# Performance work log

Hardware: AMD Instinct MI355X
Metric: run time of the kernel (lower is better)

## Reference

```python
import jax, jax.numpy as jnp
import numpy as np

HEADS = 16
WINDOW = 256
D_MODEL = 1024


def _ln(x, g, b, eps=1e-5):
    m = jnp.mean(x, -1, keepdims=True)
    var = jnp.mean((x - m) ** 2, -1, keepdims=True)
    return (x - m) * jax.lax.rsqrt(var + eps) * g + b


def _proj(x, g, b, W, bias):
    # torch: nn.Sequential(LayerNorm(d), Linear(d, h))
    return _ln(x, g, b) @ W.T + bias


def _bucket(x, pad_value):
    # x: (..., L, d) -> (..., nb, window, d), seq padded to multiple of window with pad_value
    L = x.shape[-2]
    n = WINDOW * (-(-L // WINDOW))
    pads = [(0, 0)] * x.ndim
    pads[-2] = (0, n - L)
    x = jnp.pad(x, pads, constant_values=pad_value)
    return x.reshape(*x.shape[:-2], n // WINDOW, WINDOW, x.shape[-1])


def _unfold(x, pad_value):
    # x: (..., nb, w, d) -> (..., nb, 2w, d): previous bucket (pad_value for bucket 0) || current
    pads = [(0, 0)] * x.ndim
    pads[-3] = (1, 0)
    prev = jnp.pad(x, pads, constant_values=pad_value)[..., :-1, :, :]
    return jnp.concatenate([prev, x], axis=-2)


def _rotary(x):
    # lucidrains rotary_embedding_torch default: theta=10000, interleaved pairs, positions 0..S-1 along dim -2
    S, d = x.shape[-2], x.shape[-1]
    inv = 1.0 / (10000.0 ** (jnp.arange(0, d, 2, dtype=jnp.float32) / d))
    freqs = jnp.arange(S, dtype=jnp.float32)[:, None] * inv[None, :]  # (S, d/2)
    freqs = jnp.repeat(freqs, 2, axis=-1)  # (S, d)
    cos, sin = jnp.cos(freqs).astype(x.dtype), jnp.sin(freqs).astype(x.dtype)
    xp = x.reshape(*x.shape[:-1], d // 2, 2)
    xr = jnp.stack([-xp[..., 1], xp[..., 0]], axis=-1).reshape(x.shape)
    return x * cos + xr * sin


def _forward(q, k, v, cell,
             ln_q_w, ln_q_b, w_q, b_q,
             ln_k_w, ln_k_b, w_k, b_k,
             ln_v_w, ln_v_b, w_v, b_v,
             ln_o_w, ln_o_b, w_o, b_o):
    B, L, D = q.shape
    hd = D // HEADS

    def split_heads(x):  # (B, L, D) -> (B, H, L, hd)
        return x.reshape(B, L, HEADS, hd).transpose(0, 2, 1, 3)

    qh = split_heads(_proj(q, ln_q_w, ln_q_b, w_q, b_q))
    kh = split_heads(_proj(k, ln_k_w, ln_k_b, w_k, b_k))
    vh = split_heads(_proj(v, ln_v_w, ln_v_b, w_v, b_v))

    bq = _bucket(qh, -1.0)                 # (B, H, nb, w, hd)
    bk = _unfold(_bucket(kh, -1.0), -1.0)  # (B, H, nb, 2w, hd)
    bv = _unfold(_bucket(vh, -1.0), -1.0)

    nb = bq.shape[2]
    n = nb * WINDOW
    i = _bucket(jnp.arange(n, dtype=jnp.int32)[:, None], -1)   # (nb, w, 1)
    j = jnp.swapaxes(_unfold(i, -1), -1, -2)                    # (nb, 1, 2w)
    mask = (i >= j) & (j != -1)                                 # (nb, w, 2w) causal + left pad
    req = _bucket(cell, -1)                                     # (B, 1, nb, w, 1)
    rek = jnp.swapaxes(_unfold(req, -1), -1, -2)                # (B, 1, nb, 1, 2w)
    mask = mask & (req == rek)                                  # (B, 1, nb, w, 2w)

    bq = _rotary(bq)
    bk = _rotary(bk)

    p = jnp.einsum('bhnqd,bhnkd->bhnqk', bq, bk) / jnp.sqrt(jnp.asarray(hd, bq.dtype))
    p = jnp.where(mask, p, jnp.finfo(p.dtype).min)
    a = jax.nn.softmax(p, axis=-1)
    o = jnp.einsum('bhnqk,bhnkd->bhnqd', a, bv)   # (B, H, nb, w, hd)
    o = o.reshape(B, HEADS, n, hd)[:, :, :L]      # drop seq padding
    o = o.transpose(0, 2, 1, 3).reshape(B, L, D)  # merge heads
    return _proj(o, ln_o_w, ln_o_b, w_o, b_o)


def setup_inputs() -> dict:
    key = jax.random.key(0)
    ks = jax.random.split(key, 10)
    B, L, D = 2, 4096, D_MODEL
    inp = {
        'q': jax.random.normal(ks[0], (B, L, D), dtype=jnp.float32),
        'k': jax.random.normal(ks[1], (B, L, D), dtype=jnp.float32),
        'v': jax.random.normal(ks[2], (B, L, D), dtype=jnp.float32),
        'cell': jnp.sort(jax.random.randint(ks[3], (B, 1, L, 1), 0, 64, dtype=jnp.int32), axis=2),
    }
    for idx, name in enumerate(['q', 'k', 'v', 'o']):
        inp[f'ln_{name}_w'] = jnp.ones((D,), jnp.float32)
        inp[f'ln_{name}_b'] = jnp.zeros((D,), jnp.float32)
        inp[f'w_{name}'] = jax.random.normal(ks[4 + idx], (D, D), dtype=jnp.float32) * 0.02
        inp[f'b_{name}'] = jnp.zeros((D,), jnp.float32)
    return inp


def reference(q, k, v, cell,
              ln_q_w, ln_q_b, w_q, b_q,
              ln_k_w, ln_k_b, w_k, b_k,
              ln_v_w, ln_v_b, w_v, b_v,
              ln_o_w, ln_o_b, w_o, b_o):
    return _forward(q, k, v, cell,
                    ln_q_w, ln_q_b, w_q, b_q,
                    ln_k_w, ln_k_b, w_k, b_k,
                    ln_v_w, ln_v_b, w_v, b_v,
                    ln_o_w, ln_o_b, w_o, b_o)
```

## Files before the change

kernel.cpp:

```cpp
#include <hip/hip_runtime.h>

#define HEADS 16
#define HD 64
#define DM 1024
#define LSEQ 4096
#define NEGF (-1.0e30f)

typedef __attribute__((ext_vector_type(8))) short bf16x8;
typedef __attribute__((ext_vector_type(4))) float f32x4;
typedef unsigned short u16;

#define MFMA16(a, b, c) __builtin_amdgcn_mfma_f32_16x16x32_bf16((a), (b), (c), 0, 0, 0)

static __device__ __forceinline__ float b2f(u16 u) {
  union { float f; unsigned i; } t; t.i = ((unsigned)u) << 16; return t.f;
}
static __device__ __forceinline__ u16 f2b(float f) {
  union { float f; unsigned i; } t; t.f = f;
  unsigned r = t.i + 0x7fffu + ((t.i >> 16) & 1u);
  return (u16)(r >> 16);
}
static __device__ __forceinline__ ushort4 pk4(float4 v) {
  return make_ushort4(f2b(v.x), f2b(v.y), f2b(v.z), f2b(v.w));
}
static __device__ __forceinline__ void gload16(const void* g, void* l) {
  __builtin_amdgcn_global_load_lds((const __attribute__((address_space(1))) void*)g,
                                   (__attribute__((address_space(3))) void*)l, 16, 0, 0);
}

__global__ __launch_bounds__(256) void prep(
    const float4* __restrict__ q, const float4* __restrict__ k, const float4* __restrict__ v,
    const float* __restrict__ g0, const float* __restrict__ b0,
    const float* __restrict__ g1, const float* __restrict__ b1,
    const float* __restrict__ g2, const float* __restrict__ b2,
    ushort4* __restrict__ o0, ushort4* __restrict__ o1, ushort4* __restrict__ o2,
    const float4* __restrict__ w0, const float4* __restrict__ w1,
    const float4* __restrict__ w2, const float4* __restrict__ w3,
    ushort4* __restrict__ wout,
    float* __restrict__ ropc, float* __restrict__ rops,
    const float* __restrict__ g3, const float* __restrict__ b3,
    const float* __restrict__ bias_o,
    float* __restrict__ c1, float* __restrict__ c2b) {
  __shared__ float ps[8];
  const int bid = blockIdx.x, tid = threadIdx.x;
  const int lane = tid & 63, wave = tid >> 6;
  if (bid < 24576) {
    const int row = bid & 8191, sel = bid >> 13;
    const float4* src = (sel == 0) ? q : (sel == 1) ? k : v;
    const float* gam = (sel == 0) ? g0 : (sel == 1) ? g1 : g2;
    const float* bet = (sel == 0) ? b0 : (sel == 1) ? b1 : b2;
    ushort4* dst = (sel == 0) ? o0 : (sel == 1) ? o1 : o2;

    float4 v4 = src[(size_t)row * 256 + tid];
    float s = v4.x + v4.y + v4.z + v4.w;
    float s2 = v4.x * v4.x + v4.y * v4.y + v4.z * v4.z + v4.w * v4.w;
#pragma unroll
    for (int d = 1; d < 64; d <<= 1) { s += __shfl_xor(s, d); s2 += __shfl_xor(s2, d); }
    if (lane == 0) { ps[wave] = s; ps[4 + wave] = s2; }
    __syncthreads();
    float tot = ps[0] + ps[1] + ps[2] + ps[3];
    float tot2 = ps[4] + ps[5] + ps[6] + ps[7];
    float mean = tot * (1.f / 1024.f);
    float var = tot2 * (1.f / 1024.f) - mean * mean;
    float rstd = rsqrtf(var + 1e-5f);
    float4 gv = ((const float4*)gam)[tid];
    float4 bv = ((const float4*)bet)[tid];
    dst[(size_t)row * 256 + tid] = make_ushort4(
        f2b((v4.x - mean) * rstd * gv.x + bv.x), f2b((v4.y - mean) * rstd * gv.y + bv.y),
        f2b((v4.z - mean) * rstd * gv.z + bv.z), f2b((v4.w - mean) * rstd * gv.w + bv.w));
  } else if (bid < 25600) {
    int i = (bid - 24576) * 256 + tid;
    wout[i]          = pk4(w0[i]);
    wout[i + 262144] = pk4(w1[i]);
    wout[i + 524288] = pk4(w2[i]);
    float4 wv = w3[i];
    float4 g4 = ((const float4*)g3)[i & 255];
    wv.x *= g4.x; wv.y *= g4.y; wv.z *= g4.z; wv.w *= g4.w;
    wout[i + 786432] = pk4(wv);
  } else if (bid < 25728) {
    int idx = (bid - 25600) * 256 + tid;
    int p = idx >> 6, d = idx & 63;
    int t2 = d & ~1;
    double inv = pow(10000.0, -(double)t2 / 64.0);
    double f = (double)p * inv;
    ropc[idx] = (float)cos(f);
    rops[idx] = (float)sin(f);
  } else {
    int n = bid - 25728;
    float4 wv = w3[n * 256 + tid];
    float4 gv = ((const float4*)g3)[tid];
    float4 bv = ((const float4*)b3)[tid];
    float s1 = wv.x * gv.x + wv.y * gv.y + wv.z * gv.z + wv.w * gv.w;
    float s2 = wv.x * bv.x + wv.y * bv.y + wv.z * bv.z + wv.w * bv.w;
#pragma unroll
    for (int d = 1; d < 64; d <<= 1) { s1 += __shfl_xor(s1, d); s2 += __shfl_xor(s2, d); }
    if (lane == 0) { ps[wave] = s1; ps[4 + wave] = s2; }
    __syncthreads();
    if (tid == 0) {
      c1[n] = ps[0] + ps[1] + ps[2] + ps[3];
      c2b[n] = ps[4] + ps[5] + ps[6] + ps[7] + bias_o[n];
    }
  }
}

__global__ __launch_bounds__(256) void ostats(const ushort4* __restrict__ xin,
                                              float* __restrict__ mean,
                                              float* __restrict__ rstd) {
  __shared__ float ps[8];
  int row = blockIdx.x, tid = threadIdx.x;
  int lane = tid & 63, wave = tid >> 6;
  ushort4 u = xin[(size_t)row * 256 + tid];
  float x = b2f(u.x), y = b2f(u.y), z = b2f(u.z), w = b2f(u.w);
  float s = x + y + z + w;
  float s2 = x * x + y * y + z * z + w * w;
#pragma unroll
  for (int d = 1; d < 64; d <<= 1) { s += __shfl_xor(s, d); s2 += __shfl_xor(s2, d); }
  if (lane == 0) { ps[wave] = s; ps[4 + wave] = s2; }
  __syncthreads();
  if (tid == 0) {
    float tot = ps[0] + ps[1] + ps[2] + ps[3];
    float tot2 = ps[4] + ps[5] + ps[6] + ps[7];
    float m = tot * (1.f / 1024.f);
    float var = tot2 * (1.f / 1024.f) - m * m;
    mean[row] = m;
    rstd[row] = rsqrtf(var + 1e-5f);
  }
}

__global__ __launch_bounds__(256, 3) void gemm_qkv(
    const u16* __restrict__ Aq, const u16* __restrict__ Ak, const u16* __restrict__ Av,
    const u16* __restrict__ wbf,
    const float* __restrict__ bq, const float* __restrict__ bk, const float* __restrict__ bv,
    const float* __restrict__ ropc, const float* __restrict__ rops,
    u16* __restrict__ qrot, u16* __restrict__ krot, u16* __restrict__ vTp) {
  __shared__ __align__(16) char smem[34816];
  u16* Als = (u16*)smem;
  u16* Bls = (u16*)(smem + 16384);
  const int tid = threadIdx.x, lane = tid & 63, wave = tid >> 6;
  const int g = lane >> 4, ln15 = lane & 15;
  const int mode = blockIdx.y;
  const u16* A = (mode == 0) ? Aq : (mode == 1) ? Ak : Av;
  const u16* Bw = wbf + (size_t)mode * 1048576;
  const float* bias = (mode == 0) ? bq : (mode == 1) ? bk : bv;
  const int bid = blockIdx.x;
  const int xcd = bid & 7, idx = bid >> 3;
  const int row0 = (xcd * 8 + (idx >> 3)) * 128;
  const int col0 = (idx & 7) * 128;
  const int wm = (wave >> 1) * 64, wn = (wave & 1) * 64;
  const int K = 1024;
  f32x4 acc[4][4] = {};

  for (int k0 = 0; k0 < K; k0 += 64) {
#pragma unroll
    for (int i = 0; i < 4; ++i) {
      int ch = i * 4 + wave;
      int olin = ch * 1024 + lane * 16;
      int r = olin >> 7;
      int cel = ((olin ^ ((r & 7) << 4)) >> 1) & 63;
      gload16(A + (size_t)(row0 + r) * K + k0 + cel, (char*)Als + ch * 1024);
    }
#pragma unroll
    for (int i = 0; i < 4; ++i) {
      int ch = i * 4 + wave;
      int olin = ch * 1024 + lane * 16;
      int r = olin >> 7;
      int cel = ((olin ^ ((r & 7) << 4)) >> 1) & 63;
      gload16(Bw + (size_t)(col0 + r) * K + k0 + cel, (char*)Bls + ch * 1024);
    }
    __syncthreads();
#pragma unroll
    for (int ks = 0; ks < 2; ++ks) {
      bf16x8 af[4], bfv[4];
      int cb = (ks * 32 + g * 8) * 2;
#pragma unroll
      for (int mi = 0; mi < 4; ++mi) {
        int r = wm + mi * 16 + ln15;
        af[mi] = *(const bf16x8*)((const char*)Als + r * 128 + (cb ^ ((r & 7) << 4)));
      }
#pragma unroll
      for (int ni = 0; ni < 4; ++ni) {
        int r = wn + ni * 16 + ln15;
        bfv[ni] = *(const bf16x8*)((const char*)Bls + r * 128 + (cb ^ ((r & 7) << 4)));
      }
#pragma unroll
      for (int mi = 0; mi < 4; ++mi)
#pragma unroll
        for (int ni = 0; ni < 4; ++ni)
          acc[mi][ni] = MFMA16(af[mi], bfv[ni], acc[mi][ni]);
    }
    __syncthreads();
  }

  u16* Cl = (u16*)smem;
#pragma unroll
  for (int mi = 0; mi < 4; ++mi)
#pragma unroll
    for (int ni = 0; ni < 4; ++ni)
#pragma unroll
      for (int r = 0; r < 4; ++r) {
        int rowc = wm + mi * 16 + g * 4 + r;
        int colc = wn + ni * 16 + ln15;
        int row = row0 + rowc, col = col0 + colc;
        float val = acc[mi][ni][r] + bias[col];
        if (mode == 2) {
          Cl[colc * 136 + rowc] = f2b(val);
        } else {
          if (mode == 0) val *= 0.125f;
          float oth = __shfl_xor(val, 1);
          int d = col & 63;
          int pp = (row & 255) + ((mode == 1) ? 256 : 0);
          float cc = ropc[pp * 64 + d], ss = rops[pp * 64 + d];
          Cl[rowc * 136 + colc] = f2b((d & 1) ? (val * cc + oth * ss) : (val * cc - oth * ss));
        }
      }
  __syncthreads();
  if (mode == 2) {
#pragma unroll
    for (int i = 0; i < 8; ++i) {
      int c2 = i * 256 + tid;
      int dloc = c2 >> 4, lgrp = c2 & 15;
      bf16x8 vv = *(const bf16x8*)(Cl + dloc * 136 + lgrp * 8);
      int colg = col0 + dloc, hh = colg >> 6, d = colg & 63;
      int l = row0 + lgrp * 8, bb = l >> 12, ll = l & 4095;
      *(bf16x8*)(vTp + (((size_t)bb * HEADS + hh) * HD + d) * LSEQ + ll) = vv;
    }
  } else {
    u16* dst = (mode == 0) ? qrot : krot;
#pragma unroll
    for (int i = 0; i < 8; ++i) {
      int c2 = i * 256 + tid;
      int rowc = c2 >> 4, cgrp = c2 & 15;
      bf16x8 vv = *(const bf16x8*)(Cl + rowc * 136 + cgrp * 8);
      int l = row0 + rowc, bb = l >> 12, ll = l & 4095;
      int colg = col0 + cgrp * 8, hh = colg >> 6, d0 = colg & 63;
      *(bf16x8*)(dst + (((size_t)bb * HEADS + hh) * LSEQ + ll) * HD + d0) = vv;
    }
  }
}

__global__ __launch_bounds__(256, 3) void gemm_o(
    const u16* __restrict__ A, const u16* __restrict__ Bw,
    const float* __restrict__ mean, const float* __restrict__ rstd,
    const float* __restrict__ c1, const float* __restrict__ c2b,
    float* __restrict__ outf) {
  __shared__ __align__(16) u16 Als[128 * 64];
  __shared__ __align__(16) u16 Bls[128 * 64];
  const int tid = threadIdx.x, lane = tid & 63, wave = tid >> 6;
  const int g = lane >> 4, ln15 = lane & 15;
  const int bid = blockIdx.x;
  const int xcd = bid & 7, idx = bid >> 3;
  const int row0 = (xcd * 8 + (idx >> 3)) * 128;
  const int col0 = (idx & 7) * 128;
  const int wm = (wave >> 1) * 64, wn = (wave & 1) * 64;
  const int K = 1024, N = 1024;
  f32x4 acc[4][4] = {};

  for (int k0 = 0; k0 < K; k0 += 64) {
#pragma unroll
    for (int i = 0; i < 4; ++i) {
      int ch = i * 4 + wave;
      int olin = ch * 1024 + lane * 16;
      int r = olin >> 7;
      int cel = ((olin ^ ((r & 7) << 4)) >> 1) & 63;
      gload16(A + (size_t)(row0 + r) * K + k0 + cel, (char*)Als + ch * 1024);
    }
#pragma unroll
    for (int i = 0; i < 4; ++i) {
      int ch = i * 4 + wave;
      int olin = ch * 1024 + lane * 16;
      int r = olin >> 7;
      int cel = ((olin ^ ((r & 7) << 4)) >> 1) & 63;
      gload16(Bw + (size_t)(col0 + r) * K + k0 + cel, (char*)Bls + ch * 1024);
    }
    __syncthreads();
#pragma unroll
    for (int ks = 0; ks < 2; ++ks) {
      bf16x8 af[4], bfv[4];
      int cb = (ks * 32 + g * 8) * 2;
#pragma unroll
      for (int mi = 0; mi < 4; ++mi) {
        int r = wm + mi * 16 + ln15;
        af[mi] = *(const bf16x8*)((const char*)Als + r * 128 + (cb ^ ((r & 7) << 4)));
      }
#pragma unroll
      for (int ni = 0; ni < 4; ++ni) {
        int r = wn + ni * 16 + ln15;
        bfv[ni] = *(const bf16x8*)((const char*)Bls + r * 128 + (cb ^ ((r & 7) << 4)));
      }
#pragma unroll
      for (int mi = 0; mi < 4; ++mi)
#pragma unroll
        for (int ni = 0; ni < 4; ++ni)
          acc[mi][ni] = MFMA16(af[mi], bfv[ni], acc[mi][ni]);
    }
    __syncthreads();
  }

#pragma unroll
  for (int mi = 0; mi < 4; ++mi)
#pragma unroll
    for (int r = 0; r < 4; ++r) {
      int row = row0 + wm + mi * 16 + g * 4 + r;
      float rho = rstd[row];
      float rm = rho * mean[row];
#pragma unroll
      for (int ni = 0; ni < 4; ++ni) {
        int col = col0 + wn + ni * 16 + ln15;
        outf[(size_t)row * N + col] = rho * acc[mi][ni][r] - rm * c1[col] + c2b[col];
      }
    }
}

__global__ __launch_bounds__(512, 2) void attn_kernel(
    const u16* __restrict__ qrot,
    const u16* __restrict__ krot,
    const u16* __restrict__ vT,
    const int* __restrict__ cell,
    const float* __restrict__ ropc, const float* __restrict__ rops,
    u16* __restrict__ o) {
  __shared__ __align__(16) u16 Kc[2][128 * 64];
  __shared__ __align__(16) u16 Pl[8 * 32 * 64];
  __shared__ int ci[256];
  __shared__ int cj[512];

  const int tid = threadIdx.x, lane = tid & 63, wave = tid >> 6;
  const int g = lane >> 4, ln15 = lane & 15;
  const int bucket = blockIdx.x & 15;
  const int h = (blockIdx.x >> 4) & 15;
  const int b = blockIdx.x >> 8;
  const int w0 = bucket * 256;
  const size_t base = (size_t)(b * HEADS + h) * LSEQ * HD;

  if (tid < 256) ci[tid] = cell[b * LSEQ + w0 + tid];
  {
    int gj = w0 - 256 + tid;
    cj[tid] = (gj >= 0) ? cell[b * LSEQ + gj] : (int)0x80000000;
  }

  bf16x8 qf[2][2];
#pragma unroll
  for (int mi = 0; mi < 2; ++mi)
#pragma unroll
    for (int ks = 0; ks < 2; ++ks)
      qf[mi][ks] = *(const bf16x8*)(qrot + base +
          (size_t)(w0 + wave * 32 + mi * 16 + ln15) * HD + ks * 32 + g * 8);

  bf16x8 qfB[2][2];
#pragma unroll
  for (int ks = 0; ks < 2; ++ks) {
    const int d0 = ks * 32 + g * 8;
    float rc[8], rs8[8];
#pragma unroll
    for (int j = 0; j < 8; ++j) {
      rc[j] = ropc[256 * 64 + d0 + j];
      rs8[j] = rops[256 * 64 + d0 + j];
    }
#pragma unroll
    for (int mi = 0; mi < 2; ++mi) {
      bf16x8 s = qf[mi][ks], t;
#pragma unroll
      for (int j = 0; j < 8; j += 2) {
        float e = b2f((u16)s[j]), od = b2f((u16)s[j + 1]);
        t[j]     = (short)f2b(e * rc[j] - od * rs8[j]);
        t[j + 1] = (short)f2b(e * rs8[j] + od * rc[j]);
      }
      qfB[mi][ks] = t;
    }
  }

  f32x4 Oa[2][4] = {};
  float mrow[2][4], lrow[2][4];
#pragma unroll
  for (int a1 = 0; a1 < 2; ++a1)
#pragma unroll
    for (int a2 = 0; a2 < 4; ++a2) { mrow[a1][a2] = NEGF; lrow[a1][a2] = 0.f; }

#define STAGE_K(bi, s)                                                          \
  {                                                                             \
    int gj0_ = w0 - 256 + (s) * 128;                                            \
    _Pragma("unroll")                                                           \
    for (int i_ = 0; i_ < 2; ++i_) {                                            \
      int ch_ = i_ * 8 + wave;                                                  \
      int olin_ = ch_ * 1024 + lane * 16;                                       \
      int r_ = olin_ >> 7;                                                      \
      int cel_ = ((olin_ ^ ((r_ & 7) << 4)) >> 1) & 63;                         \
      gload16(krot + base + (size_t)(gj0_ + r_) * HD + cel_,                    \
              (char*)Kc[bi] + ch_ * 1024);                                      \
    }                                                                           \
  }

  const int s0 = (bucket == 0) ? 2 : 0;
  STAGE_K(0, s0);
  __syncthreads();

  const int crb_lo = ci[0], crb_hi = ci[255];
  const int crw_lo = ci[wave * 32], crw_hi = ci[wave * 32 + 31];

  for (int s = s0; s < 4; ++s) {
    const int cur = (s - s0) & 1;
    if (s + 1 < 4) {
      int k1 = (s + 1) * 2;
      bool need = false;
#pragma unroll
      for (int kk = 0; kk < 2; ++kk) {
        int clo = cj[(k1 + kk) * 64], chi = cj[(k1 + kk) * 64 + 63];
        need = need || !(chi < crb_lo || clo > crb_hi);
      }
      if (need) STAGE_K(cur ^ 1, s + 1);
    }

#pragma unroll
    for (int sub = 0; sub < 2; ++sub) {
      const int k = s * 2 + sub;
      if (k * 64 > wave * 32 + 287) continue;
      {
        int clo = cj[k * 64], chi = cj[k * 64 + 63];
        if (chi < crw_lo || clo > crw_hi) continue;
      }
      const int gj0 = w0 - 256 + k * 64;
      const int lr0 = sub * 64;
      const bool prevhalf = (k < 4);

      bf16x8 vb[2][4];
#pragma unroll
      for (int jb = 0; jb < 2; ++jb)
#pragma unroll
        for (int nd = 0; nd < 4; ++nd) {
          int d = nd * 16 + ln15;
          int p0 = gj0 + jb * 32 + g * 8;
          vb[jb][nd] = *(const bf16x8*)(vT + base + (size_t)d * LSEQ + p0);
        }

#pragma unroll
      for (int mi = 0; mi < 2; ++mi) {
        f32x4 sc[4] = {};
        __builtin_amdgcn_s_setprio(1);
#pragma unroll
        for (int ks = 0; ks < 2; ++ks) {
          int cb = (ks * 32 + g * 8) * 2;
          bf16x8 aq = prevhalf ? qfB[mi][ks] : qf[mi][ks];
#pragma unroll
          for (int ni = 0; ni < 4; ++ni) {
            int r = lr0 + ni * 16 + ln15;
            bf16x8 kf = *(const bf16x8*)((const char*)Kc[cur] + r * 128 + (cb ^ ((r & 7) << 4)));
            sc[ni] = MFMA16(aq, kf, sc[ni]);
          }
        }
        __builtin_amdgcn_s_setprio(0);
        float mx[4] = {NEGF, NEGF, NEGF, NEGF};
#pragma unroll
        for (int ni = 0; ni < 4; ++ni)
#pragma unroll
          for (int r = 0; r < 4; ++r) {
            int iloc = wave * 32 + mi * 16 + g * 4 + r;
            int p = k * 64 + ni * 16 + ln15;
            bool ok = (p <= iloc + 256) && (ci[iloc] == cj[p]);
            float sv = ok ? sc[ni][r] : NEGF;
            sc[ni][r] = sv;
            mx[r] = fmaxf(mx[r], sv);
          }
#pragma unroll
        for (int d = 1; d < 16; d <<= 1)
#pragma unroll
          for (int r = 0; r < 4; ++r) mx[r] = fmaxf(mx[r], __shfl_xor(mx[r], d));
        float rs[4] = {0.f, 0.f, 0.f, 0.f};
        bool big = false;
#pragma unroll
        for (int r = 0; r < 4; ++r) big = big || (mx[r] > mrow[mi][r] + 8.0f);
        if (__any(big)) {
#pragma unroll
          for (int r = 0; r < 4; ++r) {
            float mold = mrow[mi][r];
            float mnew = fmaxf(mold, mx[r]);
            float alpha = __expf(mold - mnew);
            mrow[mi][r] = mnew;
            lrow[mi][r] *= alpha;
#pragma unroll
            for (int nd = 0; nd < 4; ++nd) Oa[mi][nd][r] *= alpha;
          }
        }
#pragma unroll
        for (int ni = 0; ni < 4; ++ni)
#pragma unroll
          for (int r = 0; r < 4; ++r) {
            float sv = sc[ni][r];
            float p = (sv > NEGF * 0.5f) ? __expf(sv - mrow[mi][r]) : 0.f;
            rs[r] += p;
            int row = mi * 16 + g * 4 + r;
            int colb = (ni * 16 + ln15) * 2;
            *(u16*)((char*)Pl + wave * 4096 + row * 128 + (colb ^ ((row & 7) << 4))) = f2b(p);
          }
#pragma unroll
        for (int d = 1; d < 16; d <<= 1)
#pragma unroll
          for (int r = 0; r < 4; ++r) rs[r] += __shfl_xor(rs[r], d);
#pragma unroll
        for (int r = 0; r < 4; ++r) lrow[mi][r] += rs[r];
      }

#pragma unroll
      for (int jb = 0; jb < 2; ++jb) {
        bf16x8 pa[2];
        int cb = (jb * 32 + g * 8) * 2;
#pragma unroll
        for (int mi = 0; mi < 2; ++mi) {
          int row = mi * 16 + ln15;
          pa[mi] = *(const bf16x8*)((const char*)Pl + wave * 4096 + row * 128 + (cb ^ ((row & 7) << 4)));
        }
        __builtin_amdgcn_s_setprio(1);
#pragma unroll
        for (int mi = 0; mi < 2; ++mi)
#pragma unroll
          for (int nd = 0; nd < 4; ++nd) Oa[mi][nd] = MFMA16(pa[mi], vb[jb][nd], Oa[mi][nd]);
        __builtin_amdgcn_s_setprio(0);
      }
    }

    __syncthreads();
  }

#pragma unroll
  for (int mi = 0; mi < 2; ++mi)
#pragma unroll
    for (int r = 0; r < 4; ++r) {
      float invl = 1.0f / lrow[mi][r];
      int gi = w0 + wave * 32 + mi * 16 + g * 4 + r;
      size_t ob = ((size_t)b * LSEQ + gi) * DM + h * HD;
#pragma unroll
      for (int nd = 0; nd < 4; ++nd) o[ob + nd * 16 + ln15] = f2b(Oa[mi][nd][r] * invl);
    }
#undef STAGE_K
}

extern "C" void kernel_launch(void* const* d_in, const int* in_sizes, int n_in,
                              void* d_out, int out_size, void* d_ws, size_t ws_size,
                              hipStream_t stream) {
  const float* q = (const float*)d_in[0];
  const float* k = (const float*)d_in[1];
  const float* v = (const float*)d_in[2];
  const int* cell = (const int*)d_in[3];
  const float* lnw[4] = {(const float*)d_in[4], (const float*)d_in[8], (const float*)d_in[12], (const float*)d_in[16]};
  const float* lnb[4] = {(const float*)d_in[5], (const float*)d_in[9], (const float*)d_in[13], (const float*)d_in[17]};
  const float* Wm[4]  = {(const float*)d_in[6], (const float*)d_in[10], (const float*)d_in[14], (const float*)d_in[18]};
  const float* bi[4]  = {(const float*)d_in[7], (const float*)d_in[11], (const float*)d_in[15], (const float*)d_in[19]};

  char* ws = (char*)d_ws;
  u16* xlnq  = (u16*)(ws);
  u16* wbf   = (u16*)(ws + 16777216);
  u16* qrot  = (u16*)(ws + 25165824);
  u16* krot  = (u16*)(ws + 41943040);
  float* omean = (float*)(ws + 58720256);
  float* orstd = (float*)(ws + 58753024);
  float* c1    = (float*)(ws + 58785792);
  float* c2b   = (float*)(ws + 58789888);
  u16* vT    = (u16*)(ws + 75497472);
  u16* obuf  = (u16*)(ws + 92274688);
  float* ropc = (float*)(ws + 109051904);
  float* rops = (float*)(ws + 109182976);
  u16* xlnk = obuf;
  u16* xlnv = (u16*)d_out;

  prep<<<26752, 256, 0, stream>>>(
      (const float4*)q, (const float4*)k, (const float4*)v,
      lnw[0], lnb[0], lnw[1], lnb[1], lnw[2], lnb[2],
      (ushort4*)xlnq, (ushort4*)xlnk, (ushort4*)xlnv,
      (const float4*)Wm[0], (const float4*)Wm[1], (const float4*)Wm[2], (const float4*)Wm[3],
      (ushort4*)wbf, ropc, rops,
      lnw[3], lnb[3], bi[3], c1, c2b);

  dim3 gq(512, 3);
  gemm_qkv<<<gq, 256, 0, stream>>>(xlnq, xlnk, xlnv, wbf, bi[0], bi[1], bi[2],
                                   ropc, rops, qrot, krot, vT);
  attn_kernel<<<512, 512, 0, stream>>>(qrot, krot, vT, cell, ropc, rops, obuf);
  ostats<<<8192, 256, 0, stream>>>((const ushort4*)obuf, omean, orstd);
  gemm_o<<<512, 256, 0, stream>>>(obuf, wbf + 3145728, omean, orstd, c1, c2b, (float*)d_out);
}
```

Baseline: 191.4 us.

## Split attention blocks into half-buckets, load K directly, compute row sums via MFMA

The attention kernel now launches 1024 blocks of 256 threads, each covering half a query bucket, with a blockIdx remap that groups neighbouring blocks. K is read straight from global memory instead of being double-buffered in LDS, which removes the per-stage barriers and frees shared memory for more resident blocks. The softmax switches to exp2 with log2(e) folded into the query scale. Row sums come from an extra MFMA against a vector of ones instead of shuffle reductions. The risks are redundant K/V traffic across the two halves and uncoalesced direct global K fragment loads.

```diff
diff --git a/kernel.cpp b/kernel.cpp
--- a/kernel.cpp
+++ b/kernel.cpp
@@ -205,7 +205,7 @@
         if (mode == 2) {
           Cl[colc * 136 + rowc] = f2b(val);
         } else {
-          if (mode == 0) val *= 0.125f;
+          if (mode == 0) val *= 0.18033688011112042f;
           float oth = __shfl_xor(val, 1);
           int d = col & 63;
           int pp = (row & 255) + ((mode == 1) ? 256 : 0);
@@ -311,31 +311,38 @@
     }
 }
 
-__global__ __launch_bounds__(512, 2) void attn_kernel(
+__global__ __launch_bounds__(256, 4) void attn_kernel(
     const u16* __restrict__ qrot,
     const u16* __restrict__ krot,
     const u16* __restrict__ vT,
     const int* __restrict__ cell,
     const float* __restrict__ ropc, const float* __restrict__ rops,
     u16* __restrict__ o) {
-  __shared__ __align__(16) u16 Kc[2][128 * 64];
-  __shared__ __align__(16) u16 Pl[8 * 32 * 64];
-  __shared__ int ci[256];
+  __shared__ __align__(16) u16 Pl[4 * 32 * 64];
+  __shared__ int ci[128];
   __shared__ int cj[512];
 
   const int tid = threadIdx.x, lane = tid & 63, wave = tid >> 6;
   const int g = lane >> 4, ln15 = lane & 15;
-  const int bucket = blockIdx.x & 15;
-  const int h = (blockIdx.x >> 4) & 15;
-  const int b = blockIdx.x >> 8;
+  const int lin = (blockIdx.x & 7) * 128 + (blockIdx.x >> 3);
+  const int half = lin & 1;
+  const int bucket = (lin >> 1) & 15;
+  const int h = (lin >> 5) & 15;
+  const int b = lin >> 9;
   const int w0 = bucket * 256;
+  const int r0 = half * 128;
   const size_t base = (size_t)(b * HEADS + h) * LSEQ * HD;
 
-  if (tid < 256) ci[tid] = cell[b * LSEQ + w0 + tid];
+  if (tid < 128) ci[tid] = cell[b * LSEQ + w0 + r0 + tid];
   {
-    int gj = w0 - 256 + tid;
-    cj[tid] = (gj >= 0) ? cell[b * LSEQ + gj] : (int)0x80000000;
-  }
+    int j = tid;
+#pragma unroll
+    for (int it = 0; it < 2; ++it, j += 256) {
+      int gj = w0 - 256 + j;
+      cj[j] = (gj >= 0) ? cell[b * LSEQ + gj] : (int)0x80000000;
+    }
+  }
+  __syncthreads();
 
   bf16x8 qf[2][2];
 #pragma unroll
@@ -343,7 +350,7 @@
 #pragma unroll
     for (int ks = 0; ks < 2; ++ks)
       qf[mi][ks] = *(const bf16x8*)(qrot + base +
-          (size_t)(w0 + wave * 32 + mi * 16 + ln15) * HD + ks * 32 + g * 8);
+          (size_t)(w0 + r0 + wave * 32 + mi * 16 + ln15) * HD + ks * 32 + g * 8);
 
   bf16x8 qfB[2][2];
 #pragma unroll
@@ -368,168 +375,125 @@
     }
   }
 
+  bf16x8 vones;
+#pragma unroll
+  for (int j = 0; j < 8; ++j) vones[j] = (short)0x3f80;
+
   f32x4 Oa[2][4] = {};
-  float mrow[2][4], lrow[2][4];
+  f32x4 lacc[2] = {};
+  float mrow[2][4];
 #pragma unroll
   for (int a1 = 0; a1 < 2; ++a1)
 #pragma unroll
-    for (int a2 = 0; a2 < 4; ++a2) { mrow[a1][a2] = NEGF; lrow[a1][a2] = 0.f; }
-
-#define STAGE_K(bi, s)                                                          \
-  {                                                                             \
-    int gj0_ = w0 - 256 + (s) * 128;                                            \
-    _Pragma("unroll")                                                           \
-    for (int i_ = 0; i_ < 2; ++i_) {                                            \
-      int ch_ = i_ * 8 + wave;                                                  \
-      int olin_ = ch_ * 1024 + lane * 16;                                       \
-      int r_ = olin_ >> 7;                                                      \
-      int cel_ = ((olin_ ^ ((r_ & 7) << 4)) >> 1) & 63;                         \
-      gload16(krot + base + (size_t)(gj0_ + r_) * HD + cel_,                    \
-              (char*)Kc[bi] + ch_ * 1024);                                      \
-    }                                                                           \
-  }
-
-  const int s0 = (bucket == 0) ? 2 : 0;
-  STAGE_K(0, s0);
-  __syncthreads();
-
-  const int crb_lo = ci[0], crb_hi = ci[255];
+    for (int a2 = 0; a2 < 4; ++a2) mrow[a1][a2] = NEGF;
+
   const int crw_lo = ci[wave * 32], crw_hi = ci[wave * 32 + 31];
-
-  for (int s = s0; s < 4; ++s) {
-    const int cur = (s - s0) & 1;
-    if (s + 1 < 4) {
-      int k1 = (s + 1) * 2;
-      bool need = false;
-#pragma unroll
-      for (int kk = 0; kk < 2; ++kk) {
-        int clo = cj[(k1 + kk) * 64], chi = cj[(k1 + kk) * 64 + 63];
-        need = need || !(chi < crb_lo || clo > crb_hi);
-      }
-      if (need) STAGE_K(cur ^ 1, s + 1);
-    }
-
-#pragma unroll
-    for (int sub = 0; sub < 2; ++sub) {
-      const int k = s * 2 + sub;
-      if (k * 64 > wave * 32 + 287) continue;
-      {
-        int clo = cj[k * 64], chi = cj[k * 64 + 63];
-        if (chi < crw_lo || clo > crw_hi) continue;
-      }
-      const int gj0 = w0 - 256 + k * 64;
-      const int lr0 = sub * 64;
-      const bool prevhalf = (k < 4);
-
-      bf16x8 vb[2][4];
-#pragma unroll
-      for (int jb = 0; jb < 2; ++jb)
-#pragma unroll
-        for (int nd = 0; nd < 4; ++nd) {
-          int d = nd * 16 + ln15;
-          int p0 = gj0 + jb * 32 + g * 8;
-          vb[jb][nd] = *(const bf16x8*)(vT + base + (size_t)d * LSEQ + p0);
+  const int k0c = (bucket == 0) ? 4 : 0;
+
+  for (int k = k0c; k < 8; ++k) {
+    if (k * 64 > r0 + wave * 32 + 287) break;
+    {
+      int clo = cj[k * 64], chi = cj[k * 64 + 63];
+      if (chi < crw_lo || clo > crw_hi) continue;
+    }
+    const int gj0 = w0 - 256 + k * 64;
+    const bool prevhalf = (k < 4);
+
+#pragma unroll
+    for (int mi = 0; mi < 2; ++mi) {
+      f32x4 sc[4] = {};
+      __builtin_amdgcn_s_setprio(1);
+#pragma unroll
+      for (int ks = 0; ks < 2; ++ks) {
+        bf16x8 aq = prevhalf ? qfB[mi][ks] : qf[mi][ks];
+#pragma unroll
+        for (int ni = 0; ni < 4; ++ni) {
+          bf16x8 kf = *(const bf16x8*)(krot + base +
+              (size_t)(gj0 + ni * 16 + ln15) * HD + ks * 32 + g * 8);
+          sc[ni] = MFMA16(aq, kf, sc[ni]);
         }
-
+      }
+      __builtin_amdgcn_s_setprio(0);
+      float mx[4] = {NEGF, NEGF, NEGF, NEGF};
+#pragma unroll
+      for (int ni = 0; ni < 4; ++ni)
+#pragma unroll
+        for (int r = 0; r < 4; ++r) {
+          int rblk = wave * 32 + mi * 16 + g * 4 + r;
+          int iloc = r0 + rblk;
+          int p = k * 64 + ni * 16 + ln15;
+          bool ok = (p <= iloc + 256) && (ci[rblk] == cj[p]);
+          float sv = ok ? sc[ni][r] : NEGF;
+          sc[ni][r] = sv;
+          mx[r] = fmaxf(mx[r], sv);
+        }
+#pragma unroll
+      for (int d = 1; d < 16; d <<= 1)
+#pragma unroll
+        for (int r = 0; r < 4; ++r) mx[r] = fmaxf(mx[r], __shfl_xor(mx[r], d));
+      bool big = false;
+#pragma unroll
+      for (int r = 0; r < 4; ++r) big = big || (mx[r] > mrow[mi][r] + 8.0f);
+      if (__any(big)) {
+#pragma unroll
+        for (int r = 0; r < 4; ++r) {
+          float mold = mrow[mi][r];
+          float mnew = fmaxf(mold, mx[r]);
+          float alpha = exp2f(mold - mnew);
+          mrow[mi][r] = mnew;
+          lacc[mi][r] *= alpha;
+#pragma unroll
+          for (int nd = 0; nd < 4; ++nd) Oa[mi][nd][r] *= alpha;
+        }
+      }
+#pragma unroll
+      for (int ni = 0; ni < 4; ++ni)
+#pragma unroll
+        for (int r = 0; r < 4; ++r) {
+          float sv = sc[ni][r];
+          float p = (sv > NEGF * 0.5f) ? exp2f(sv - mrow[mi][r]) : 0.f;
+          int row = mi * 16 + g * 4 + r;
+          int colb = (ni * 16 + ln15) * 2;
+          *(u16*)((char*)Pl + wave * 4096 + row * 128 + (colb ^ ((row & 7) << 4))) = f2b(p);
+        }
+    }
+
+#pragma unroll
+    for (int jb = 0; jb < 2; ++jb) {
+      bf16x8 pa[2], vb[4];
+      int cb = (jb * 32 + g * 8) * 2;
 #pragma unroll
       for (int mi = 0; mi < 2; ++mi) {
-        f32x4 sc[4] = {};
-        __builtin_amdgcn_s_setprio(1);
-#pragma unroll
-        for (int ks = 0; ks < 2; ++ks) {
-          int cb = (ks * 32 + g * 8) * 2;
-          bf16x8 aq = prevhalf ? qfB[mi][ks] : qf[mi][ks];
-#pragma unroll
-          for (int ni = 0; ni < 4; ++ni) {
-            int r = lr0 + ni * 16 + ln15;
-            bf16x8 kf = *(const bf16x8*)((const char*)Kc[cur] + r * 128 + (cb ^ ((r & 7) << 4)));
-            sc[ni] = MFMA16(aq, kf, sc[ni]);
-          }
-        }
-        __builtin_amdgcn_s_setprio(0);
-        float mx[4] = {NEGF, NEGF, NEGF, NEGF};
-#pragma unroll
-        for (int ni = 0; ni < 4; ++ni)
-#pragma unroll
-          for (int r = 0; r < 4; ++r) {
-            int iloc = wave * 32 + mi * 16 + g * 4 + r;
-            int p = k * 64 + ni * 16 + ln15;
-            bool ok = (p <= iloc + 256) && (ci[iloc] == cj[p]);
-            float sv = ok ? sc[ni][r] : NEGF;
-            sc[ni][r] = sv;
-            mx[r] = fmaxf(mx[r], sv);
-          }
-#pragma unroll
-        for (int d = 1; d < 16; d <<= 1)
-#pragma unroll
-          for (int r = 0; r < 4; ++r) mx[r] = fmaxf(mx[r], __shfl_xor(mx[r], d));
-        float rs[4] = {0.f, 0.f, 0.f, 0.f};
-        bool big = false;
-#pragma unroll
-        for (int r = 0; r < 4; ++r) big = big || (mx[r] > mrow[mi][r] + 8.0f);
-        if (__any(big)) {
-#pragma unroll
-          for (int r = 0; r < 4; ++r) {
-            float mold = mrow[mi][r];
-            float mnew = fmaxf(mold, mx[r]);
-            float alpha = __expf(mold - mnew);
-            mrow[mi][r] = mnew;
-            lrow[mi][r] *= alpha;
-#pragma unroll
-            for (int nd = 0; nd < 4; ++nd) Oa[mi][nd][r] *= alpha;
-          }
-        }
-#pragma unroll
-        for (int ni = 0; ni < 4; ++ni)
-#pragma unroll
-          for (int r = 0; r < 4; ++r) {
-            float sv = sc[ni][r];
-            float p = (sv > NEGF * 0.5f) ? __expf(sv - mrow[mi][r]) : 0.f;
-            rs[r] += p;
-            int row = mi * 16 + g * 4 + r;
-            int colb = (ni * 16 + ln15) * 2;
-            *(u16*)((char*)Pl + wave * 4096 + row * 128 + (colb ^ ((row & 7) << 4))) = f2b(p);
-          }
-#pragma unroll
-        for (int d = 1; d < 16; d <<= 1)
-#pragma unroll
-          for (int r = 0; r < 4; ++r) rs[r] += __shfl_xor(rs[r], d);
-#pragma unroll
-        for (int r = 0; r < 4; ++r) lrow[mi][r] += rs[r];
-      }
-
-#pragma unroll
-      for (int jb = 0; jb < 2; ++jb) {
-        bf16x8 pa[2];
-        int cb = (jb * 32 + g * 8) * 2;
-#pragma unroll
-        for (int mi = 0; mi < 2; ++mi) {
-          int row = mi * 16 + ln15;
-          pa[mi] = *(const bf16x8*)((const char*)Pl + wave * 4096 + row * 128 + (cb ^ ((row & 7) << 4)));
-        }
-        __builtin_amdgcn_s_setprio(1);
-#pragma unroll
-        for (int mi = 0; mi < 2; ++mi)
-#pragma unroll
-          for (int nd = 0; nd < 4; ++nd) Oa[mi][nd] = MFMA16(pa[mi], vb[jb][nd], Oa[mi][nd]);
-        __builtin_amdgcn_s_setprio(0);
-      }
-    }
-
-    __syncthreads();
+        int row = mi * 16 + ln15;
+        pa[mi] = *(const bf16x8*)((const char*)Pl + wave * 4096 + row * 128 + (cb ^ ((row & 7) << 4)));
+      }
+#pragma unroll
+      for (int nd = 0; nd < 4; ++nd) {
+        int d = nd * 16 + ln15;
+        int p0 = gj0 + jb * 32 + g * 8;
+        vb[nd] = *(const bf16x8*)(vT + base + (size_t)d * LSEQ + p0);
+      }
+      __builtin_amdgcn_s_setprio(1);
+#pragma unroll
+      for (int mi = 0; mi < 2; ++mi) {
+#pragma unroll
+        for (int nd = 0; nd < 4; ++nd) Oa[mi][nd] = MFMA16(pa[mi], vb[nd], Oa[mi][nd]);
+        lacc[mi] = MFMA16(pa[mi], vones, lacc[mi]);
+      }
+      __builtin_amdgcn_s_setprio(0);
+    }
   }
 
 #pragma unroll
   for (int mi = 0; mi < 2; ++mi)
 #pragma unroll
     for (int r = 0; r < 4; ++r) {
-      float invl = 1.0f / lrow[mi][r];
-      int gi = w0 + wave * 32 + mi * 16 + g * 4 + r;
+      float invl = 1.0f / lacc[mi][r];
+      int gi = w0 + r0 + wave * 32 + mi * 16 + g * 4 + r;
       size_t ob = ((size_t)b * LSEQ + gi) * DM + h * HD;
 #pragma unroll
       for (int nd = 0; nd < 4; ++nd) o[ob + nd * 16 + ln15] = f2b(Oa[mi][nd][r] * invl);
     }
-#undef STAGE_K
 }
 
 extern "C" void kernel_launch(void* const* d_in, const int* in_sizes, int n_in,
@@ -571,7 +535,7 @@
   dim3 gq(512, 3);
   gemm_qkv<<<gq, 256, 0, stream>>>(xlnq, xlnk, xlnv, wbf, bi[0], bi[1], bi[2],
                                    ropc, rops, qrot, krot, vT);
-  attn_kernel<<<512, 512, 0, stream>>>(qrot, krot, vT, cell, ropc, rops, obuf);
+  attn_kernel<<<1024, 256, 0, stream>>>(qrot, krot, vT, cell, ropc, rops, obuf);
   ostats<<<8192, 256, 0, stream>>>((const ushort4*)obuf, omean, orstd);
   gemm_o<<<512, 256, 0, stream>>>(obuf, wbf + 3145728, omean, orstd, c1, c2b, (float*)d_out);
 }
```

New measurement: 250.4 us. 30.8% more time.
